# Optimization experiments

Measured on AMD Instinct MI355X. Metric: run time of the kernel, lower is better.

## Reference

```python
import jax, jax.numpy as jnp
import numpy as np

EMBED_DIM = 1024
NUM_HEADS = 16
HEAD_DIM = EMBED_DIM // NUM_HEADS
ROPE_BASE = 10000.0


def _rope_cos_sin(seq_len, head_dim, dtype=jnp.float32):
    inv_freq = 1.0 / (ROPE_BASE ** (jnp.arange(0, head_dim, 2, dtype=jnp.float32) / head_dim))
    t = jnp.arange(seq_len, dtype=jnp.float32)
    freqs = jnp.outer(t, inv_freq)            # [N, D/2]
    emb = jnp.concatenate([freqs, freqs], -1)  # [N, D]
    return jnp.cos(emb).astype(dtype), jnp.sin(emb).astype(dtype)


def _rotate_half(x):
    x1, x2 = jnp.split(x, 2, axis=-1)
    return jnp.concatenate([-x2, x1], axis=-1)


def setup_inputs() -> dict:
    key = jax.random.key(0)
    k1, k2, k3 = jax.random.split(key, 3)
    B, N, C = 2, 2048, EMBED_DIM
    x = jax.random.normal(k1, (B, N, C), jnp.float32)
    Wqkv = jax.random.normal(k2, (3 * C, C), jnp.float32) * (C ** -0.5)
    Wout = jax.random.normal(k3, (C, C), jnp.float32) * (C ** -0.5)
    bout = jnp.zeros((C,), jnp.float32)
    return {"x": x, "Wqkv": Wqkv, "Wout": Wout, "bout": bout}


def reference(x, Wqkv, Wout, bout):
    B, N, C = x.shape
    H, D = NUM_HEADS, HEAD_DIM
    qkv = jnp.einsum('bnc,fc->bnf', x, Wqkv)          # [B,N,3C]
    qkv = qkv.reshape(B, N, 3, H, D).transpose(2, 0, 3, 1, 4)  # [3,B,H,N,D]
    q, k, v = qkv[0], qkv[1], qkv[2]
    cos, sin = _rope_cos_sin(N, D, x.dtype)           # [N,D]
    cos = cos[None, None]
    sin = sin[None, None]
    q = q * cos + _rotate_half(q) * sin
    k = k * cos + _rotate_half(k) * sin
    scale = D ** -0.5
    scores = jnp.einsum('bhqd,bhkd->bhqk', q, k) * scale
    attn = jax.nn.softmax(scores, axis=-1)
    out = jnp.einsum('bhqk,bhkd->bhqd', attn, v)      # [B,H,N,D]
    out = out.transpose(0, 2, 1, 3).reshape(B, N, C)
    return jnp.einsum('bnc,oc->bno', out, Wout) + bout
```

## Files before the change

kernel.cpp:

```cpp
#include <hip/hip_runtime.h>
#include <stdint.h>

#define DI __device__ __forceinline__

typedef __attribute__((ext_vector_type(8))) __bf16 bf16x8;
typedef __attribute__((ext_vector_type(8))) short short8;
typedef __attribute__((ext_vector_type(4))) float f32x4;
typedef __attribute__((ext_vector_type(16))) float f32x16;

DI unsigned short f2bf(float f) {
    union { float f; uint32_t u; } v; v.f = f;
    uint32_t r = v.u + 0x7FFFu + ((v.u >> 16) & 1u);
    return (unsigned short)(r >> 16);
}
DI uint32_t pk2(float a, float b) {
    uint32_t r;
    asm("v_cvt_pk_bf16_f32 %0, %1, %2" : "=v"(r) : "v"(a), "v"(b));
    return r;
}
DI bf16x8 asb(short8 s) { union { short8 s; bf16x8 b; } u; u.s = s; return u.b; }
DI bf16x8 asb4(uint32_t a, uint32_t b, uint32_t c, uint32_t d) {
    union { uint32_t u[4]; bf16x8 b; } x; x.u[0] = a; x.u[1] = b; x.u[2] = c; x.u[3] = d; return x.b;
}
DI void gload16(const void* g, void* l) {
    __builtin_amdgcn_global_load_lds(
        (const __attribute__((address_space(1))) void*)g,
        (__attribute__((address_space(3))) void*)l, 16, 0, 0);
}
DI int swzc(int c) { return c ^ ((c >> 3) & 7); }

__global__ __launch_bounds__(256) void prepk(
    const float* __restrict__ x, const float* __restrict__ Wqkv,
    const float* __restrict__ Wout,
    unsigned short* __restrict__ xb, unsigned short* __restrict__ wqkvb,
    unsigned short* __restrict__ woutb,
    float* __restrict__ cosT, float* __restrict__ sinT) {
    const int bid = blockIdx.x, tid = threadIdx.x;
    if (bid < 8192) {
        const float* in; unsigned short* out; int i;
        if (bid < 4096)      { in = x;    out = xb;    i = bid * 256 + tid; }
        else if (bid < 7168) { in = Wqkv; out = wqkvb; i = (bid - 4096) * 256 + tid; }
        else                 { in = Wout; out = woutb; i = (bid - 7168) * 256 + tid; }
        float4 v = ((const float4*)in)[i];
        union { unsigned short u[4]; uint2 q; } p;
        p.u[0] = f2bf(v.x); p.u[1] = f2bf(v.y); p.u[2] = f2bf(v.z); p.u[3] = f2bf(v.w);
        ((uint2*)out)[i] = p.q;
    } else {
        int i = (bid - 8192) * 256 + tid;
        int n = i >> 5, d = i & 31;
        float inv = powf(10000.0f, -(float)(2 * d) * (1.0f / 64.0f));
        float a = (float)n * inv;
        float s, c;
        sincosf(a, &s, &c);
        cosT[i] = c; sinT[i] = s;
    }
}

template <int MODE, int BM>
__global__ __launch_bounds__(256) void gemm_bt(
    const unsigned short* __restrict__ A, const unsigned short* __restrict__ Bt,
    int M, int N, int K,
    unsigned short* __restrict__ Qbuf, unsigned short* __restrict__ Kbuf,
    unsigned short* __restrict__ Vt,
    const float* __restrict__ cosT, const float* __restrict__ sinT,
    float* __restrict__ Cout, const float* __restrict__ bias) {
    constexpr int WM = BM / 2;
    constexpr int MI = WM / 16;
    __shared__ __align__(16) unsigned short As[BM * 32];
    __shared__ __align__(16) unsigned short Bs[128 * 32];
    const int tid = threadIdx.x;
    const int wave = tid >> 6, lane = tid & 63, g = lane >> 4, li = lane & 15;
    const int wr = wave >> 1, wc = wave & 1;
    const int m0 = blockIdx.y * BM, n0 = blockIdx.x * 128;

    f32x4 acc[MI][4] = {};
    const int nK = K >> 5;
    for (int kk = 0; kk < nK; ++kk) {
#pragma unroll
        for (int i = 0; i < BM / 64; ++i) {
            int cb = i * 256 + wave * 64;
            int c = cb + lane;
            int r = c >> 2, k0 = (c & 3) * 8;
            gload16(A + (size_t)(m0 + r) * K + kk * 32 + k0, &As[cb * 8]);
        }
#pragma unroll
        for (int i = 0; i < 2; ++i) {
            int cb = i * 256 + wave * 64;
            int c = cb + lane;
            int r = c >> 2, k0 = (c & 3) * 8;
            gload16(Bt + (size_t)(n0 + r) * K + kk * 32 + k0, &Bs[cb * 8]);
        }
        __syncthreads();
        short8 af[MI], bf[4];
#pragma unroll
        for (int mi = 0; mi < MI; ++mi)
            af[mi] = *(const short8*)&As[(wr * WM + mi * 16 + li) * 32 + g * 8];
#pragma unroll
        for (int ni = 0; ni < 4; ++ni)
            bf[ni] = *(const short8*)&Bs[(wc * 64 + ni * 16 + li) * 32 + g * 8];
#pragma unroll
        for (int mi = 0; mi < MI; ++mi)
#pragma unroll
            for (int ni = 0; ni < 4; ++ni)
                acc[mi][ni] = __builtin_amdgcn_mfma_f32_16x16x32_bf16(
                    asb(af[mi]), asb(bf[ni]), acc[mi][ni], 0, 0, 0);
        __syncthreads();
    }

    if (MODE == 1) {
#pragma unroll
        for (int mi = 0; mi < MI; ++mi) {
            int row = m0 + wr * WM + mi * 16 + 4 * g;
#pragma unroll
            for (int ni = 0; ni < 4; ++ni) {
                int col = n0 + wc * 64 + ni * 16 + li;
                float b = bias[col];
#pragma unroll
                for (int r = 0; r < 4; ++r)
                    Cout[(size_t)(row + r) * N + col] = acc[mi][ni][r] + b;
            }
        }
    } else {
        const int fb = n0 + wc * 64;
        const int three = fb >> 10;
        const int hh = (fb & 1023) >> 6;
        const int bq = m0 >> 11;
        const int nb0 = m0 & 2047;
        const size_t bh = (size_t)(bq * 16 + hh);
        if (three < 2) {
#pragma unroll
            for (int mi = 0; mi < MI; ++mi) {
#pragma unroll
                for (int r = 0; r < 4; ++r) {
                    int n = nb0 + wr * WM + mi * 16 + 4 * g + r;
                    float v0 = acc[mi][0][r], v1 = acc[mi][1][r];
                    float v2 = acc[mi][2][r], v3 = acc[mi][3][r];
                    float c0 = cosT[n * 32 + li],      s0 = sinT[n * 32 + li];
                    float c1 = cosT[n * 32 + 16 + li], s1 = sinT[n * 32 + 16 + li];
                    float o0 = v0 * c0 - v2 * s0;
                    float o2 = v2 * c0 + v0 * s0;
                    float o1 = v1 * c1 - v3 * s1;
                    float o3 = v3 * c1 + v1 * s1;
                    if (three == 0) {
                        const float qs = 0.18033688f;
                        o0 *= qs; o1 *= qs; o2 *= qs; o3 *= qs;
                    }
                    unsigned short* dst = (three == 0 ? Qbuf : Kbuf) + (bh * 2048 + n) * 64;
                    dst[li] = f2bf(o0); dst[16 + li] = f2bf(o1);
                    dst[32 + li] = f2bf(o2); dst[48 + li] = f2bf(o3);
                }
            }
        } else {
            unsigned short* vtw = As + wave * 1024;
            const int gsw = ((g & 1) << 1) | (g >> 1);
#pragma unroll
            for (int mi = 0; mi < MI; ++mi) {
                __syncthreads();
#pragma unroll
                for (int ni = 0; ni < 4; ++ni)
#pragma unroll
                    for (int r = 0; r < 4; ++r)
                        vtw[(ni * 16 + li) * 16 + 4 * gsw + r] = f2bf(acc[mi][ni][r]);
                __syncthreads();
                uint4 lo = *(const uint4*)&vtw[lane * 16];
                uint4 hi = *(const uint4*)&vtw[lane * 16 + 8];
                int nbase = nb0 + wr * WM + mi * 16;
                unsigned short* dst = Vt + (bh * 64 + lane) * 2048 + nbase;
                *(uint4*)dst = lo;
                *(uint4*)(dst + 8) = hi;
            }
        }
    }
}

__global__ __launch_bounds__(256) void attnk(
    const unsigned short* __restrict__ Qb, const unsigned short* __restrict__ Kb,
    const unsigned short* __restrict__ Vt, unsigned short* __restrict__ Obuf) {
    __shared__ __align__(16) unsigned short Ks[2][64 * 64];
    __shared__ __align__(16) unsigned short Vs[2][64 * 64];
    const int tid = threadIdx.x, wave = tid >> 6, lane = tid & 63;
    const int h = lane >> 5, li = lane & 31;

    const int fid = blockIdx.y * 16 + blockIdx.x;
    const int logical = (fid & 7) * 64 + (fid >> 3);
    const int bh = logical >> 4, qt = logical & 15;
    const int q0 = qt * 128 + wave * 32;

    bf16x8 qf[4];
    const unsigned short* qp = Qb + ((size_t)bh * 2048 + q0 + li) * 64;
#pragma unroll
    for (int c = 0; c < 4; ++c) qf[c] = asb(*(const short8*)(qp + c * 16 + h * 8));

    const uint4* kg = (const uint4*)(Kb + (size_t)bh * 2048 * 64);
    const uint4* vg = (const uint4*)Vt;
    const int r0 = tid >> 3, r1 = (tid + 256) >> 3, cc = tid & 7;
    const int sw0 = swzc(tid) * 8, sw1 = swzc(tid + 256) * 8;
    const size_t vrow0 = ((size_t)bh * 64 + r0) * 256 + cc;
    const size_t vrow1 = ((size_t)bh * 64 + r1) * 256 + cc;

    uint4 kr0, kr1, vr0, vr1;

    f32x16 o0 = {}, o1 = {};
    float l_ = 0.f;

    kr0 = kg[tid]; kr1 = kg[256 + tid];
    vr0 = vg[vrow0]; vr1 = vg[vrow1];
    *(uint4*)&Ks[0][sw0] = kr0; *(uint4*)&Ks[0][sw1] = kr1;
    *(uint4*)&Vs[0][sw0] = vr0; *(uint4*)&Vs[0][sw1] = vr1;
    __syncthreads();
    kr0 = kg[512 + tid]; kr1 = kg[512 + 256 + tid];
    vr0 = vg[vrow0 + 8]; vr1 = vg[vrow1 + 8];

    for (int kt = 0; kt < 32; ++kt) {
        const int cur = kt & 1;

        f32x16 s0 = {}, s1 = {};
#pragma unroll
        for (int c = 0; c < 4; ++c) {
            int ch = 2 * c + h;
            bf16x8 k0 = asb(*(const short8*)&Ks[cur][li * 64 + ((ch ^ (li & 7)) * 8)]);
            bf16x8 k1 = asb(*(const short8*)&Ks[cur][(32 + li) * 64 + ((ch ^ (li & 7)) * 8)]);
            s0 = __builtin_amdgcn_mfma_f32_32x32x16_bf16(k0, qf[c], s0, 0, 0, 0);
            s1 = __builtin_amdgcn_mfma_f32_32x32x16_bf16(k1, qf[c], s1, 0, 0, 0);
        }

        float sm0 = 0.f, sm1 = 0.f;
#pragma unroll
        for (int r = 0; r < 16; ++r) {
            float p0 = __builtin_exp2f(s0[r]); s0[r] = p0; sm0 += p0;
            float p1 = __builtin_exp2f(s1[r]); s1[r] = p1; sm1 += p1;
        }
        l_ += sm0 + sm1;

        uint32_t w0[8], w1[8];
#pragma unroll
        for (int m = 0; m < 8; ++m) {
            w0[m] = pk2(s0[2 * m], s0[2 * m + 1]);
            w1[m] = pk2(s1[2 * m], s1[2 * m + 1]);
        }

#pragma unroll
        for (int ks = 0; ks < 4; ++ks) {
            const uint32_t* wk = (ks < 2) ? w0 : w1;
            const int sub = (ks & 1) * 4;
            bf16x8 pf = asb4(wk[sub], wk[sub + 1], wk[sub + 2], wk[sub + 3]);
            int ch = 2 * ks + h;
            bf16x8 vf0 = asb(*(const short8*)&Vs[cur][li * 64 + ((ch ^ (li & 7)) * 8)]);
            bf16x8 vf1 = asb(*(const short8*)&Vs[cur][(32 + li) * 64 + ((ch ^ (li & 7)) * 8)]);
            o0 = __builtin_amdgcn_mfma_f32_32x32x16_bf16(pf, vf0, o0, 0, 0, 0);
            o1 = __builtin_amdgcn_mfma_f32_32x32x16_bf16(pf, vf1, o1, 0, 0, 0);
        }

        if (kt < 31) {
            const int nxt = cur ^ 1;
            *(uint4*)&Ks[nxt][sw0] = kr0; *(uint4*)&Ks[nxt][sw1] = kr1;
            *(uint4*)&Vs[nxt][sw0] = vr0; *(uint4*)&Vs[nxt][sw1] = vr1;
            __syncthreads();
            if (kt < 30) {
                int nt = kt + 2;
                kr0 = kg[nt * 512 + tid]; kr1 = kg[nt * 512 + 256 + tid];
                vr0 = vg[vrow0 + nt * 8]; vr1 = vg[vrow1 + nt * 8];
            }
        }
    }

    float lfull = l_ + __shfl_xor(l_, 32);
    float linv = 1.0f / lfull;
    const int b = bh >> 4, hh = bh & 15;
#pragma unroll
    for (int r = 0; r < 16; ++r) {
        int qrow = (r & 3) + 8 * (r >> 2) + 4 * h;
        float lr = __shfl(linv, qrow);
        int n = q0 + qrow;
        unsigned short* dst = Obuf + ((size_t)(b * 2048 + n)) * 1024 + hh * 64 + li;
        dst[0]  = f2bf(o0[r] * lr);
        dst[32] = f2bf(o1[r] * lr);
    }
}

extern "C" void kernel_launch(void* const* d_in, const int* in_sizes, int n_in,
                              void* d_out, int out_size, void* d_ws, size_t ws_size,
                              hipStream_t stream) {
    const float* x    = (const float*)d_in[0];
    const float* Wqkv = (const float*)d_in[1];
    const float* Wout = (const float*)d_in[2];
    const float* bout = (const float*)d_in[3];
    float* out = (float*)d_out;
    char* ws = (char*)d_ws;

    size_t off = 0;
    unsigned short* xb    = (unsigned short*)(ws + off);
    unsigned short* Obuf  = xb;
    off += (size_t)4096 * 1024 * 2;
    unsigned short* wqkvb = (unsigned short*)(ws + off); off += (size_t)3072 * 1024 * 2;
    unsigned short* woutb = (unsigned short*)(ws + off); off += (size_t)1024 * 1024 * 2;
    float* cosT = (float*)(ws + off); off += (size_t)2048 * 32 * 4;
    float* sinT = (float*)(ws + off); off += (size_t)2048 * 32 * 4;
    unsigned short* Qbuf = (unsigned short*)(ws + off); off += (size_t)32 * 2048 * 64 * 2;
    unsigned short* Kbuf = (unsigned short*)(ws + off); off += (size_t)32 * 2048 * 64 * 2;
    unsigned short* Vt   = (unsigned short*)(ws + off); off += (size_t)32 * 64 * 2048 * 2;

    prepk<<<8448, 256, 0, stream>>>(x, Wqkv, Wout, xb, wqkvb, woutb, cosT, sinT);

    gemm_bt<0, 128><<<dim3(24, 32), 256, 0, stream>>>(
        xb, wqkvb, 4096, 3072, 1024, Qbuf, Kbuf, Vt, cosT, sinT, nullptr, nullptr);

    attnk<<<dim3(16, 32), 256, 0, stream>>>(Qbuf, Kbuf, Vt, Obuf);

    gemm_bt<1, 64><<<dim3(8, 64), 256, 0, stream>>>(
        Obuf, woutb, 4096, 1024, 1024, nullptr, nullptr, nullptr, nullptr, nullptr,
        out, bout);
}
```

Measured before the change: 205.7 us.

## Split attention KV range into two halves with a separate combine kernel

Splits each attention block's key/value sweep into two halves processed by separate workgroups, doubling the grid from 512 to 1024 blocks. Each half writes unnormalized bf16 partial outputs and row sums to workspace. A new combine kernel then adds the partials and normalizes into the layout the output GEMM expects. The goal is better occupancy across the CUs. The cost is an extra launch, extra global traffic for the partials, and an extra bf16 rounding of the partial outputs. The softmax has no max subtraction, so summing the partials is exact.

```diff
diff --git a/kernel.cpp b/kernel.cpp
--- a/kernel.cpp
+++ b/kernel.cpp
@@ -18,6 +18,8 @@
     asm("v_cvt_pk_bf16_f32 %0, %1, %2" : "=v"(r) : "v"(a), "v"(b));
     return r;
 }
+DI float bflo(uint32_t w) { union { uint32_t u; float f; } x; x.u = w << 16; return x.f; }
+DI float bfhi(uint32_t w) { union { uint32_t u; float f; } x; x.u = w & 0xffff0000u; return x.f; }
 DI bf16x8 asb(short8 s) { union { short8 s; bf16x8 b; } u; u.s = s; return u.b; }
 DI bf16x8 asb4(uint32_t a, uint32_t b, uint32_t c, uint32_t d) {
     union { uint32_t u[4]; bf16x8 b; } x; x.u[0] = a; x.u[1] = b; x.u[2] = c; x.u[3] = d; return x.b;
@@ -175,15 +177,18 @@
 
 __global__ __launch_bounds__(256) void attnk(
     const unsigned short* __restrict__ Qb, const unsigned short* __restrict__ Kb,
-    const unsigned short* __restrict__ Vt, unsigned short* __restrict__ Obuf) {
+    const unsigned short* __restrict__ Vt, unsigned short* __restrict__ Op,
+    float* __restrict__ lp) {
     __shared__ __align__(16) unsigned short Ks[2][64 * 64];
     __shared__ __align__(16) unsigned short Vs[2][64 * 64];
     const int tid = threadIdx.x, wave = tid >> 6, lane = tid & 63;
     const int h = lane >> 5, li = lane & 31;
 
-    const int fid = blockIdx.y * 16 + blockIdx.x;
-    const int logical = (fid & 7) * 64 + (fid >> 3);
-    const int bh = logical >> 4, qt = logical & 15;
+    const int fid = blockIdx.y * 32 + blockIdx.x;
+    const int logical = (fid & 7) * 128 + (fid >> 3);
+    const int bh = logical >> 5;
+    const int s  = (logical >> 4) & 1;
+    const int qt = logical & 15;
     const int q0 = qt * 128 + wave * 32;
 
     bf16x8 qf[4];
@@ -191,12 +196,12 @@
 #pragma unroll
     for (int c = 0; c < 4; ++c) qf[c] = asb(*(const short8*)(qp + c * 16 + h * 8));
 
-    const uint4* kg = (const uint4*)(Kb + (size_t)bh * 2048 * 64);
+    const uint4* kg = (const uint4*)(Kb + (size_t)bh * 2048 * 64) + (size_t)s * 16 * 512;
     const uint4* vg = (const uint4*)Vt;
     const int r0 = tid >> 3, r1 = (tid + 256) >> 3, cc = tid & 7;
     const int sw0 = swzc(tid) * 8, sw1 = swzc(tid + 256) * 8;
-    const size_t vrow0 = ((size_t)bh * 64 + r0) * 256 + cc;
-    const size_t vrow1 = ((size_t)bh * 64 + r1) * 256 + cc;
+    const size_t vrow0 = ((size_t)bh * 64 + r0) * 256 + cc + (size_t)s * 16 * 8;
+    const size_t vrow1 = ((size_t)bh * 64 + r1) * 256 + cc + (size_t)s * 16 * 8;
 
     uint4 kr0, kr1, vr0, vr1;
 
@@ -211,8 +216,8 @@
     kr0 = kg[512 + tid]; kr1 = kg[512 + 256 + tid];
     vr0 = vg[vrow0 + 8]; vr1 = vg[vrow1 + 8];
 
-    for (int kt = 0; kt < 32; ++kt) {
-        const int cur = kt & 1;
+    for (int kti = 0; kti < 16; ++kti) {
+        const int cur = kti & 1;
 
         f32x16 s0 = {}, s1 = {};
 #pragma unroll
@@ -251,31 +256,47 @@
             o1 = __builtin_amdgcn_mfma_f32_32x32x16_bf16(pf, vf1, o1, 0, 0, 0);
         }
 
-        if (kt < 31) {
+        if (kti < 15) {
             const int nxt = cur ^ 1;
             *(uint4*)&Ks[nxt][sw0] = kr0; *(uint4*)&Ks[nxt][sw1] = kr1;
             *(uint4*)&Vs[nxt][sw0] = vr0; *(uint4*)&Vs[nxt][sw1] = vr1;
             __syncthreads();
-            if (kt < 30) {
-                int nt = kt + 2;
+            if (kti < 14) {
+                int nt = kti + 2;
                 kr0 = kg[nt * 512 + tid]; kr1 = kg[nt * 512 + 256 + tid];
                 vr0 = vg[vrow0 + nt * 8]; vr1 = vg[vrow1 + nt * 8];
             }
         }
     }
 
-    float lfull = l_ + __shfl_xor(l_, 32);
-    float linv = 1.0f / lfull;
-    const int b = bh >> 4, hh = bh & 15;
+    const size_t obase = ((size_t)s * 32 + bh) * 2048;
 #pragma unroll
     for (int r = 0; r < 16; ++r) {
         int qrow = (r & 3) + 8 * (r >> 2) + 4 * h;
-        float lr = __shfl(linv, qrow);
         int n = q0 + qrow;
-        unsigned short* dst = Obuf + ((size_t)(b * 2048 + n)) * 1024 + hh * 64 + li;
-        dst[0]  = f2bf(o0[r] * lr);
-        dst[32] = f2bf(o1[r] * lr);
-    }
+        unsigned short* dst = Op + (obase + n) * 64 + li;
+        dst[0]  = f2bf(o0[r]);
+        dst[32] = f2bf(o1[r]);
+    }
+    float lc = l_ + __shfl_xor(l_, 32);
+    if (h == 0) lp[obase + q0 + li] = lc;
+}
+
+__global__ __launch_bounds__(256) void combk(
+    const unsigned short* __restrict__ Op, const float* __restrict__ lp,
+    unsigned short* __restrict__ Obuf) {
+    int t = blockIdx.x * 256 + threadIdx.x;
+    int d8 = t & 7, hh = (t >> 3) & 15, n = (t >> 7) & 2047, b = t >> 18;
+    size_t row = ((size_t)(b * 16 + hh)) * 2048 + n;
+    float linv = 1.0f / (lp[row] + lp[row + 65536]);
+    const uint4 a = *(const uint4*)(Op + row * 64 + d8 * 8);
+    const uint4 c = *(const uint4*)(Op + 4194304 + row * 64 + d8 * 8);
+    uint4 o;
+    o.x = pk2(linv * (bflo(a.x) + bflo(c.x)), linv * (bfhi(a.x) + bfhi(c.x)));
+    o.y = pk2(linv * (bflo(a.y) + bflo(c.y)), linv * (bfhi(a.y) + bfhi(c.y)));
+    o.z = pk2(linv * (bflo(a.z) + bflo(c.z)), linv * (bfhi(a.z) + bfhi(c.z)));
+    o.w = pk2(linv * (bflo(a.w) + bflo(c.w)), linv * (bfhi(a.w) + bfhi(c.w)));
+    *(uint4*)(Obuf + ((size_t)(b * 2048 + n)) * 1024 + hh * 64 + d8 * 8) = o;
 }
 
 extern "C" void kernel_launch(void* const* d_in, const int* in_sizes, int n_in,
@@ -299,13 +320,17 @@
     unsigned short* Qbuf = (unsigned short*)(ws + off); off += (size_t)32 * 2048 * 64 * 2;
     unsigned short* Kbuf = (unsigned short*)(ws + off); off += (size_t)32 * 2048 * 64 * 2;
     unsigned short* Vt   = (unsigned short*)(ws + off); off += (size_t)32 * 64 * 2048 * 2;
+    unsigned short* Op   = (unsigned short*)(ws + off); off += (size_t)2 * 32 * 2048 * 64 * 2;
+    float* lp            = (float*)(ws + off);          off += (size_t)2 * 32 * 2048 * 4;
 
     prepk<<<8448, 256, 0, stream>>>(x, Wqkv, Wout, xb, wqkvb, woutb, cosT, sinT);
 
     gemm_bt<0, 128><<<dim3(24, 32), 256, 0, stream>>>(
         xb, wqkvb, 4096, 3072, 1024, Qbuf, Kbuf, Vt, cosT, sinT, nullptr, nullptr);
 
-    attnk<<<dim3(16, 32), 256, 0, stream>>>(Qbuf, Kbuf, Vt, Obuf);
+    attnk<<<dim3(32, 32), 256, 0, stream>>>(Qbuf, Kbuf, Vt, Op, lp);
+
+    combk<<<2048, 256, 0, stream>>>(Op, lp, Obuf);
 
     gemm_bt<1, 64><<<dim3(8, 64), 256, 0, stream>>>(
         Obuf, woutb, 4096, 1024, 1024, nullptr, nullptr, nullptr, nullptr, nullptr,
```

Result: slower. 212.8 us (+3.5%).
